# Kernel tuning notes

Measured on AMD Instinct MI355X. Metric: run time of the kernel, lower is better.

The kernel has to match this reference:

```python
import jax, jax.numpy as jnp
import numpy as np

N = 131072
K = 1024
D = 64

def setup_inputs() -> dict:
    key = jax.random.key(0)
    k1, k2 = jax.random.split(key)
    x = jax.random.normal(k1, (N, D), dtype=jnp.float32)
    emb_weight = jax.random.normal(k2, (K, D), dtype=jnp.float32)
    return {"x": x, "emb_weight": emb_weight}

def reference(x, emb_weight):
    distances = (
        jnp.sum(x * x, axis=1, keepdims=True)
        + jnp.sum(emb_weight * emb_weight, axis=1)
        - 2.0 * jnp.matmul(x, emb_weight.T)
    )
    codebook_indices = jnp.argmin(distances, axis=1)  # [N]
    probs = jax.nn.one_hot(codebook_indices, K, dtype=x.dtype)  # [N, K]
    z_q = emb_weight[codebook_indices]  # [N, D]
    return (z_q, probs)
```

## Files before the change

kernel.cpp:

```cpp
#include <hip/hip_runtime.h>
#include <math.h>

#define N_TOK 131072
#define K_CB  1024
#define D_DIM 64
#define MARGIN_U 72u

#define WS_EN     0
#define WS_ES     4096
#define WS_CNT    266240
#define WS_LIST   266256

typedef short bf16x8 __attribute__((ext_vector_type(8)));
typedef float f32x4  __attribute__((ext_vector_type(4)));

__device__ __forceinline__ ushort f2bf(float f) {
    uint u = __float_as_uint(f);
    u += 0x7FFFu + ((u >> 16) & 1u);
    return (ushort)(u >> 16);
}
__device__ __forceinline__ float bf2f(ushort h) {
    return __uint_as_float(((uint)h) << 16);
}

__global__ __launch_bounds__(256) void prep_kernel(
    const float* __restrict__ emb, float* __restrict__ en,
    ushort* __restrict__ es, uint* __restrict__ fixcnt)
{
    const int tid = threadIdx.x;
    const int pb  = blockIdx.x;
    const int c6  = tid & 63;
    const int q   = tid >> 6;
    const int code = pb * 64 + c6;
    if (pb == 0 && tid == 0) *fixcnt = 0;

    const int cb = code >> 4, jj = code & 15;
    const float* er = emb + (size_t)code * D_DIM;
    #pragma unroll
    for (int j = 0; j < 16; ++j) {
        int d = q * 16 + j;
        float f = er[d];
        ushort h = f2bf(f);
        ushort l = f2bf(f - bf2f(h));
        int ks = d >> 5, quad = (d >> 3) & 3, e = d & 7;
        es[(size_t)(((cb * 4 + ks)     * 4 + quad) * 16 + jj) * 8 + e] = h;
        es[(size_t)(((cb * 4 + ks + 2) * 4 + quad) * 16 + jj) * 8 + e] = l;
    }
    if (q == 0) {
        float s = 0.f;
        #pragma unroll
        for (int d = 0; d < D_DIM; ++d) s = fmaf(er[d], er[d], s);
        en[code] = s;
    }
}

__global__ __launch_bounds__(256) void vq_onehot(
    const float* __restrict__ x, const float* __restrict__ emb,
    const float* __restrict__ en, const ushort* __restrict__ es,
    float* __restrict__ zq, float* __restrict__ probs,
    uint* __restrict__ fixcnt, uint* __restrict__ fixlist, uint fixcap)
{
    const int tid  = threadIdx.x;
    const int wave = tid >> 6, lane = tid & 63;
    const int quad = lane >> 4, l15 = lane & 15;
    const int rg = wave >> 1;
    const int h  = wave & 1;
    const int blockRow = blockIdx.x * 64;
    const int waveRowBase = blockRow + rg * 32;

    __shared__ uint lds_b1[2][64];
    __shared__ uint lds_b2[2][64];
    __shared__ int  lds_bk[64];

    bf16x8 af[2][4];
    #pragma unroll
    for (int g = 0; g < 2; ++g) {
        const float* xr = x + (size_t)(waveRowBase + g * 16 + l15) * D_DIM + quad * 8;
        f32x4 p0 = *(const f32x4*)(xr);
        f32x4 p1 = *(const f32x4*)(xr + 4);
        f32x4 p2 = *(const f32x4*)(xr + 32);
        f32x4 p3 = *(const f32x4*)(xr + 36);
        float v0[8], v1[8];
        #pragma unroll
        for (int j = 0; j < 4; ++j) { v0[j] = p0[j]; v0[4 + j] = p1[j]; v1[j] = p2[j]; v1[4 + j] = p3[j]; }
        #pragma unroll
        for (int j = 0; j < 8; ++j) {
            ushort h0 = f2bf(v0[j]);
            af[g][0][j] = (short)h0;
            af[g][2][j] = (short)f2bf(v0[j] - bf2f(h0));
            ushort h1 = f2bf(v1[j]);
            af[g][1][j] = (short)h1;
            af[g][3][j] = (short)f2bf(v1[j] - bf2f(h1));
        }
    }

    uint b1u[8], b2u[8];
    #pragma unroll
    for (int s = 0; s < 8; ++s) { b1u[s] = 0xFFFFFFFFu; b2u[s] = 0xFFFFFFFFu; }

    const bf16x8* __restrict__ esv = (const bf16x8*)es;
    const int fidx = quad * 16 + l15;
    const int cb0  = h * 32;

    bf16x8 bc[4]; float enc;
    #pragma unroll
    for (int ks = 0; ks < 4; ++ks) bc[ks] = esv[(size_t)cb0 * 256 + ks * 64 + fidx];
    enc = fmaf(en[cb0 * 16 + l15], 2048.f, 1048576.f);

    const f32x4 zv = {0.f, 0.f, 0.f, 0.f};
    f32x4* pz0 = (f32x4*)probs + (size_t)blockRow * 256 + (size_t)wave * 128 + lane * 2;

    #pragma unroll 2
    for (int i = 0; i < 32; ++i) {
        const int cb  = cb0 + i;
        const int nbi = cb0 + ((i + 1) & 31);
        bf16x8 bn[4]; float enn;
        #pragma unroll
        for (int ks = 0; ks < 4; ++ks) bn[ks] = esv[(size_t)nbi * 256 + ks * 64 + fidx];
        enn = fmaf(en[nbi * 16 + l15], 2048.f, 1048576.f);

        {
            f32x4* pz = pz0 + (size_t)i * 512;
            __builtin_nontemporal_store(zv, pz);
            __builtin_nontemporal_store(zv, pz + 1);
        }

        f32x4 acc0 = {0.f, 0.f, 0.f, 0.f};
        f32x4 acc1 = {0.f, 0.f, 0.f, 0.f};
        acc0 = __builtin_amdgcn_mfma_f32_16x16x32_bf16(af[0][0], bc[0], acc0, 0, 0, 0);
        acc0 = __builtin_amdgcn_mfma_f32_16x16x32_bf16(af[0][1], bc[1], acc0, 0, 0, 0);
        acc0 = __builtin_amdgcn_mfma_f32_16x16x32_bf16(af[0][0], bc[2], acc0, 0, 0, 0);
        acc0 = __builtin_amdgcn_mfma_f32_16x16x32_bf16(af[0][1], bc[3], acc0, 0, 0, 0);
        acc0 = __builtin_amdgcn_mfma_f32_16x16x32_bf16(af[0][2], bc[0], acc0, 0, 0, 0);
        acc0 = __builtin_amdgcn_mfma_f32_16x16x32_bf16(af[0][3], bc[1], acc0, 0, 0, 0);
        acc1 = __builtin_amdgcn_mfma_f32_16x16x32_bf16(af[1][0], bc[0], acc1, 0, 0, 0);
        acc1 = __builtin_amdgcn_mfma_f32_16x16x32_bf16(af[1][1], bc[1], acc1, 0, 0, 0);
        acc1 = __builtin_amdgcn_mfma_f32_16x16x32_bf16(af[1][0], bc[2], acc1, 0, 0, 0);
        acc1 = __builtin_amdgcn_mfma_f32_16x16x32_bf16(af[1][1], bc[3], acc1, 0, 0, 0);
        acc1 = __builtin_amdgcn_mfma_f32_16x16x32_bf16(af[1][2], bc[0], acc1, 0, 0, 0);
        acc1 = __builtin_amdgcn_mfma_f32_16x16x32_bf16(af[1][3], bc[1], acc1, 0, 0, 0);

        const uint code = (uint)(cb * 16 + l15);
        #pragma unroll
        for (int r = 0; r < 4; ++r) {
            {
                float f = fmaf(-4096.f, acc0[r], enc);
                uint u = ((uint)f << 10) | code;
                uint lo = min(b1u[r], u), hi = max(b1u[r], u);
                b1u[r] = lo; b2u[r] = min(b2u[r], hi);
            }
            {
                int s = 4 + r;
                float f = fmaf(-4096.f, acc1[r], enc);
                uint u = ((uint)f << 10) | code;
                uint lo = min(b1u[s], u), hi = max(b1u[s], u);
                b1u[s] = lo; b2u[s] = min(b2u[s], hi);
            }
        }

        #pragma unroll
        for (int ks = 0; ks < 4; ++ks) bc[ks] = bn[ks];
        enc = enn;
    }

    #pragma unroll
    for (int s = 0; s < 8; ++s) {
        #pragma unroll
        for (int off = 1; off < 16; off <<= 1) {
            uint o1 = (uint)__shfl_xor((int)b1u[s], off);
            uint o2 = (uint)__shfl_xor((int)b2u[s], off);
            uint lo = min(b1u[s], o1), hi = max(b1u[s], o1);
            b1u[s] = lo;
            b2u[s] = min(min(b2u[s], o2), hi);
        }
    }

    if (l15 == 0) {
        #pragma unroll
        for (int s = 0; s < 8; ++s) {
            int idx = rg * 32 + (s >> 2) * 16 + quad * 4 + (s & 3);
            lds_b1[h][idx] = b1u[s];
            lds_b2[h][idx] = b2u[s];
        }
    }
    __syncthreads();

    if (tid < 64) {
        uint a1 = lds_b1[0][tid], a2 = lds_b2[0][tid];
        uint c1 = lds_b1[1][tid], c2 = lds_b2[1][tid];
        uint m1 = min(a1, c1);
        uint m2 = min(min(a2, c2), max(a1, c1));
        int  mk = (int)(m1 & 1023u);
        lds_bk[tid] = mk;
        probs[(size_t)(blockRow + tid) * K_CB + mk] = 1.0f;
        if ((m2 >> 10) - (m1 >> 10) <= MARGIN_U) {
            uint idx = atomicAdd(fixcnt, 1u);
            if (idx < fixcap) fixlist[idx] = (uint)(blockRow + tid) | ((uint)mk << 17);
        }
    }
    __syncthreads();

    #pragma unroll
    for (int mb = 0; mb < 4; ++mb) {
        int rl = wave * 16 + mb * 4 + quad;
        int bk = lds_bk[rl];
        f32x4 v = ((const f32x4*)(emb + (size_t)bk * D_DIM))[l15];
        __builtin_nontemporal_store(v, (f32x4*)(zq + (size_t)(blockRow + rl) * D_DIM) + l15);
    }
}

__global__ __launch_bounds__(256) void vq_fixup(
    const float* __restrict__ x, const float* __restrict__ emb,
    const float* __restrict__ en,
    float* __restrict__ zq, float* __restrict__ probs,
    const uint* __restrict__ fixcnt, const uint* __restrict__ fixlist, uint fixcap)
{
    const int lane = threadIdx.x & 63;
    const int quad = lane >> 4, l15 = lane & 15;
    const uint gwave = (uint)((blockIdx.x * 256 + threadIdx.x) >> 6);
    uint cnt = *fixcnt;
    if (cnt > fixcap) cnt = fixcap;

    for (uint e = gwave; e < cnt; e += 4096u) {
        uint w = fixlist[e];
        int row = (int)(w & 0x1FFFFu);
        int kg  = (int)(w >> 17);

        const f32x4* xr4 = (const f32x4*)(x + (size_t)row * D_DIM) + quad * 4;
        f32x4 xv[4];
        #pragma unroll
        for (int c = 0; c < 4; ++c) xv[c] = xr4[c];
        float xn = 0.f;
        #pragma unroll
        for (int c = 0; c < 4; ++c)
            #pragma unroll
            for (int j = 0; j < 4; ++j) xn = fmaf(xv[c][j], xv[c][j], xn);
        xn += __shfl_xor(xn, 16);
        xn += __shfl_xor(xn, 32);

        float bd = INFINITY; int bk = 0;
        #pragma unroll 2
        for (int t = 0; t < 64; ++t) {
            int code = t * 16 + l15;
            const f32x4* er4 = (const f32x4*)(emb + (size_t)code * D_DIM) + quad * 4;
            float dot = 0.f;
            #pragma unroll
            for (int c = 0; c < 4; ++c) {
                f32x4 ev = er4[c];
                #pragma unroll
                for (int j = 0; j < 4; ++j) dot = fmaf(xv[c][j], ev[j], dot);
            }
            dot += __shfl_xor(dot, 16);
            dot += __shfl_xor(dot, 32);
            float dist = fmaf(-2.f, dot, xn + en[code]);
            if (dist < bd) { bd = dist; bk = code; }
        }
        #pragma unroll
        for (int off = 1; off < 16; off <<= 1) {
            float od = __shfl_xor(bd, off);
            int   ok = __shfl_xor(bk, off);
            if (od < bd || (od == bd && ok < bk)) { bd = od; bk = ok; }
        }
        if (bk != kg) {
            if (lane == 0) {
                probs[(size_t)row * K_CB + kg] = 0.f;
                probs[(size_t)row * K_CB + bk] = 1.f;
            }
            if (lane < 16)
                ((f32x4*)(zq + (size_t)row * D_DIM))[lane] =
                    ((const f32x4*)(emb + (size_t)bk * D_DIM))[lane];
        }
    }
}

extern "C" void kernel_launch(void* const* d_in, const int* in_sizes, int n_in,
                              void* d_out, int out_size, void* d_ws, size_t ws_size,
                              hipStream_t stream) {
    const float* x   = (const float*)d_in[0];
    const float* emb = (const float*)d_in[1];
    float* zq    = (float*)d_out;
    float* probs = (float*)d_out + (size_t)N_TOK * D_DIM;

    char* ws = (char*)d_ws;
    float*  en      = (float*)(ws + WS_EN);
    ushort* es      = (ushort*)(ws + WS_ES);
    uint*   fixcnt  = (uint*)(ws + WS_CNT);
    uint*   fixlist = (uint*)(ws + WS_LIST);
    uint fixcap = (ws_size > WS_LIST + 4) ? (uint)((ws_size - WS_LIST) / 4) : 0u;

    prep_kernel<<<16, 256, 0, stream>>>(emb, en, es, fixcnt);
    vq_onehot<<<N_TOK / 64, 256, 0, stream>>>(x, emb, en, es, zq, probs, fixcnt, fixlist, fixcap);
    vq_fixup<<<1024, 256, 0, stream>>>(x, emb, en, zq, probs, fixcnt, fixlist, fixcap);
}
```

Measured before the change: 744.7 us.

## Restructure probs zero-fill, vectorize codebook prep, shrink fixup margin and grid

Zeroing of the probs rows moves out of the MFMA loop. Even blocks write their zero rows before the loop and scatter the 1.0 afterwards, while odd blocks write full one-hot rows at the end. Non-temporal stores are replaced with regular stores. The prep kernel now writes hi/lo bf16 split rows as 8-wide vectors over 32 blocks. The fixup margin drops from 72 to 20, which shrinks the fix list but risks missing near-tie rows whose bf16 approximation error exceeds the new margin. The fixup grid is also reduced and one unroll pragma is removed.

```diff
diff --git a/kernel.cpp b/kernel.cpp
--- a/kernel.cpp
+++ b/kernel.cpp
@@ -4,7 +4,7 @@
 #define N_TOK 131072
 #define K_CB  1024
 #define D_DIM 64
-#define MARGIN_U 72u
+#define MARGIN_U 20u
 
 #define WS_EN     0
 #define WS_ES     4096
@@ -28,29 +28,40 @@
     ushort* __restrict__ es, uint* __restrict__ fixcnt)
 {
     const int tid = threadIdx.x;
-    const int pb  = blockIdx.x;
-    const int c6  = tid & 63;
-    const int q   = tid >> 6;
-    const int code = pb * 64 + c6;
-    if (pb == 0 && tid == 0) *fixcnt = 0;
-
-    const int cb = code >> 4, jj = code & 15;
-    const float* er = emb + (size_t)code * D_DIM;
-    #pragma unroll
-    for (int j = 0; j < 16; ++j) {
-        int d = q * 16 + j;
-        float f = er[d];
+    const int b   = blockIdx.x;
+    if (b == 0 && tid == 0) *fixcnt = 0;
+
+    const int half = tid >> 7;
+    const int t    = tid & 127;
+    const int cb   = b * 2 + half;
+    const int jj   = t & 15;
+    const int quad = (t >> 4) & 3;
+    const int ks   = (t >> 6) & 1;
+    const int code = cb * 16 + jj;
+
+    const float* er = emb + (size_t)code * D_DIM + ks * 32 + quad * 8;
+    f32x4 pa = *(const f32x4*)(er);
+    f32x4 pb = *(const f32x4*)(er + 4);
+
+    bf16x8 hi, lo;
+    #pragma unroll
+    for (int j = 0; j < 8; ++j) {
+        float f = (j < 4) ? pa[j] : pb[j - 4];
         ushort h = f2bf(f);
-        ushort l = f2bf(f - bf2f(h));
-        int ks = d >> 5, quad = (d >> 3) & 3, e = d & 7;
-        es[(size_t)(((cb * 4 + ks)     * 4 + quad) * 16 + jj) * 8 + e] = h;
-        es[(size_t)(((cb * 4 + ks + 2) * 4 + quad) * 16 + jj) * 8 + e] = l;
-    }
-    if (q == 0) {
+        hi[j] = (short)h;
+        lo[j] = (short)f2bf(f - bf2f(h));
+    }
+    bf16x8* out = (bf16x8*)es;
+    out[(size_t)(cb * 4 + ks)     * 64 + quad * 16 + jj] = hi;
+    out[(size_t)(cb * 4 + ks + 2) * 64 + quad * 16 + jj] = lo;
+
+    if (tid < 32) {
+        const int c2 = b * 32 + tid;
+        const float* e2 = emb + (size_t)c2 * D_DIM;
         float s = 0.f;
         #pragma unroll
-        for (int d = 0; d < D_DIM; ++d) s = fmaf(er[d], er[d], s);
-        en[code] = s;
+        for (int d = 0; d < D_DIM; ++d) s = fmaf(e2[d], e2[d], s);
+        en[c2] = s;
     }
 }
 
@@ -67,6 +78,7 @@
     const int h  = wave & 1;
     const int blockRow = blockIdx.x * 64;
     const int waveRowBase = blockRow + rg * 32;
+    const bool pre = (blockIdx.x & 1) == 0;
 
     __shared__ uint lds_b1[2][64];
     __shared__ uint lds_b2[2][64];
@@ -107,8 +119,15 @@
     for (int ks = 0; ks < 4; ++ks) bc[ks] = esv[(size_t)cb0 * 256 + ks * 64 + fidx];
     enc = fmaf(en[cb0 * 16 + l15], 2048.f, 1048576.f);
 
-    const f32x4 zv = {0.f, 0.f, 0.f, 0.f};
-    f32x4* pz0 = (f32x4*)probs + (size_t)blockRow * 256 + (size_t)wave * 128 + lane * 2;
+    if (pre) {
+        const f32x4 zv = {0.f, 0.f, 0.f, 0.f};
+        for (int m = 0; m < 16; ++m) {
+            float* prow = probs + (size_t)(blockRow + wave * 16 + m) * K_CB;
+            #pragma unroll
+            for (int s = 0; s < 4; ++s)
+                *(f32x4*)(prow + s * 256 + lane * 4) = zv;
+        }
+    }
 
     #pragma unroll 2
     for (int i = 0; i < 32; ++i) {
@@ -118,12 +137,6 @@
         #pragma unroll
         for (int ks = 0; ks < 4; ++ks) bn[ks] = esv[(size_t)nbi * 256 + ks * 64 + fidx];
         enn = fmaf(en[nbi * 16 + l15], 2048.f, 1048576.f);
-
-        {
-            f32x4* pz = pz0 + (size_t)i * 512;
-            __builtin_nontemporal_store(zv, pz);
-            __builtin_nontemporal_store(zv, pz + 1);
-        }
 
         f32x4 acc0 = {0.f, 0.f, 0.f, 0.f};
         f32x4 acc1 = {0.f, 0.f, 0.f, 0.f};
@@ -192,7 +205,6 @@
         uint m2 = min(min(a2, c2), max(a1, c1));
         int  mk = (int)(m1 & 1023u);
         lds_bk[tid] = mk;
-        probs[(size_t)(blockRow + tid) * K_CB + mk] = 1.0f;
         if ((m2 >> 10) - (m1 >> 10) <= MARGIN_U) {
             uint idx = atomicAdd(fixcnt, 1u);
             if (idx < fixcap) fixlist[idx] = (uint)(blockRow + tid) | ((uint)mk << 17);
@@ -205,7 +217,28 @@
         int rl = wave * 16 + mb * 4 + quad;
         int bk = lds_bk[rl];
         f32x4 v = ((const f32x4*)(emb + (size_t)bk * D_DIM))[l15];
-        __builtin_nontemporal_store(v, (f32x4*)(zq + (size_t)(blockRow + rl) * D_DIM) + l15);
+        ((f32x4*)(zq + (size_t)(blockRow + rl) * D_DIM))[l15] = v;
+    }
+
+    if (pre) {
+        if (tid < 64)
+            probs[(size_t)(blockRow + tid) * K_CB + lds_bk[tid]] = 1.0f;
+    } else {
+        for (int m = 0; m < 16; ++m) {
+            int rl = wave * 16 + m;
+            int bk = lds_bk[rl];
+            float* prow = probs + (size_t)(blockRow + rl) * K_CB;
+            #pragma unroll
+            for (int s = 0; s < 4; ++s) {
+                int c = s * 256 + lane * 4;
+                f32x4 v;
+                v[0] = (c     == bk) ? 1.f : 0.f;
+                v[1] = (c + 1 == bk) ? 1.f : 0.f;
+                v[2] = (c + 2 == bk) ? 1.f : 0.f;
+                v[3] = (c + 3 == bk) ? 1.f : 0.f;
+                *(f32x4*)(prow + c) = v;
+            }
+        }
     }
 }
 
@@ -221,7 +254,7 @@
     uint cnt = *fixcnt;
     if (cnt > fixcap) cnt = fixcap;
 
-    for (uint e = gwave; e < cnt; e += 4096u) {
+    for (uint e = gwave; e < cnt; e += 1024u) {
         uint w = fixlist[e];
         int row = (int)(w & 0x1FFFFu);
         int kg  = (int)(w >> 17);
@@ -239,7 +272,6 @@
         xn += __shfl_xor(xn, 32);
 
         float bd = INFINITY; int bk = 0;
-        #pragma unroll 2
         for (int t = 0; t < 64; ++t) {
             int code = t * 16 + l15;
             const f32x4* er4 = (const f32x4*)(emb + (size_t)code * D_DIM) + quad * 4;
@@ -288,7 +320,7 @@
     uint*   fixlist = (uint*)(ws + WS_LIST);
     uint fixcap = (ws_size > WS_LIST + 4) ? (uint)((ws_size - WS_LIST) / 4) : 0u;
 
-    prep_kernel<<<16, 256, 0, stream>>>(emb, en, es, fixcnt);
+    prep_kernel<<<32, 256, 0, stream>>>(emb, en, es, fixcnt);
     vq_onehot<<<N_TOK / 64, 256, 0, stream>>>(x, emb, en, es, zq, probs, fixcnt, fixlist, fixcap);
-    vq_fixup<<<1024, 256, 0, stream>>>(x, emb, en, zq, probs, fixcnt, fixlist, fixcap);
-}
+    vq_fixup<<<256, 256, 0, stream>>>(x, emb, en, zq, probs, fixcnt, fixlist, fixcap);
+}
```

Result: faster. 632.8 us (-15.0%).
